# Kernel tuning notes

Measured on AMD Instinct MI355X. Metric: run time of the kernel, lower is better.

## Reference

```python
import jax, jax.numpy as jnp
import numpy as np

B, N = 8, 2048
CLIP, D, BD, NC = 512, 256, 128, 10  # CLIP_EMBED_DIM, GNN_NODE_DIM, BOTTLENECK_DIM_GNN, NUM_CLASSES
LN_EPS = 1e-5


def _layer_norm(x, g, b):
    mu = jnp.mean(x, axis=-1, keepdims=True)
    var = jnp.mean(jnp.square(x - mu), axis=-1, keepdims=True)
    return (x - mu) / jnp.sqrt(var + LN_EPS) * g + b


def setup_inputs() -> dict:
    key = jax.random.key(0)
    ks = jax.random.split(key, 16)
    def w(k, shape, fan_in):
        lim = 1.0 / np.sqrt(fan_in)
        return jax.random.uniform(k, shape, jnp.float32, -lim, lim)
    return {
        "local_feat": jax.random.normal(ks[0], (B, N, CLIP), jnp.float32),
        "coords": jax.random.uniform(ks[1], (B, N, 2), jnp.float32),
        "mask": jax.random.randint(ks[2], (B, N), 0, 2).astype(bool),
        # node_encoder: Linear(CLIP->D) + LayerNorm(D)
        "enc_w": w(ks[3], (CLIP, D), CLIP), "enc_b": jnp.zeros((D,), jnp.float32),
        "enc_g": jnp.ones((D,), jnp.float32), "enc_beta": jnp.zeros((D,), jnp.float32),
        "gamma": jnp.asarray(5.0, jnp.float32),  # spatial_gamma
        "wq": w(ks[4], (D, D), D), "bq": jnp.zeros((D,), jnp.float32),
        "wk": w(ks[5], (D, D), D), "bk": jnp.zeros((D,), jnp.float32),
        "wv": w(ks[6], (D, D), D), "bv": jnp.zeros((D,), jnp.float32),
        # bottleneck: Linear(D->BD) + LayerNorm(BD)
        "bn_w": w(ks[7], (D, BD), D), "bn_b": jnp.zeros((BD,), jnp.float32),
        "bn_g": jnp.ones((BD,), jnp.float32), "bn_beta": jnp.zeros((BD,), jnp.float32),
        # classifier: Linear(BD->BD//2) + ReLU + Linear(BD//2->NC)
        "c1_w": w(ks[8], (BD, BD // 2), BD), "c1_b": jnp.zeros((BD // 2,), jnp.float32),
        "c2_w": w(ks[9], (BD // 2, NC), BD // 2), "c2_b": jnp.zeros((NC,), jnp.float32),
    }


def reference(local_feat, coords, mask, enc_w, enc_b, enc_g, enc_beta, gamma,
              wq, bq, wk, bk, wv, bv, bn_w, bn_b, bn_g, bn_beta,
              c1_w, c1_b, c2_w, c2_b):
    # node encoder: Linear + LN + ReLU -> h [B,N,D]
    h = jax.nn.relu(_layer_norm(local_feat @ enc_w + enc_b, enc_g, enc_beta))
    # pairwise euclidean distances on 2D coords (torch.cdist, under no_grad)
    xy = coords[:, :, :2]
    sq = jnp.sum(xy * xy, axis=-1)                                   # [B,N]
    d2 = sq[:, :, None] + sq[:, None, :] - 2.0 * jnp.einsum('bnd,bmd->bnm', xy, xy)
    dist = jax.lax.stop_gradient(jnp.sqrt(jnp.maximum(d2, 0.0)))     # [B,N,N]
    spatial_adj = jnp.exp(-dist * jnp.abs(gamma))
    q, k, v = h @ wq + bq, h @ wk + bk, h @ wv + bv
    scores = jnp.einsum('bnd,bmd->bnm', q, k) / jnp.sqrt(jnp.float32(D))
    attn = jax.nn.softmax(scores, axis=-1) * spatial_adj             # gated attention
    attn = jnp.where(mask[:, None, :], 0.0, attn)                    # zero masked keys
    agg = jnp.einsum('bnm,bmd->bnd', attn, v)                        # [B,N,D]
    out = jax.nn.relu(_layer_norm(agg @ bn_w + bn_b, bn_g, bn_beta)) # [B,N,BD]
    mask_v = (~mask)[:, :, None].astype(out.dtype)                   # [B,N,1]
    pooled = (out * mask_v).sum(axis=1) / jnp.maximum(mask_v.sum(axis=1), 1e-9)
    logits = jax.nn.relu(pooled @ c1_w + c1_b) @ c2_w + c2_b
    return logits, pooled
```

## Files before the change

### kernel.cpp

```cpp
#include <hip/hip_runtime.h>
#include <hip/hip_bf16.h>

typedef unsigned short ushort_t;
typedef __attribute__((ext_vector_type(8))) short s8;
typedef __attribute__((ext_vector_type(4))) float f4;
typedef __attribute__((ext_vector_type(16))) float f16v;

__device__ __forceinline__ unsigned short f2bf(float f) {
  union { float f; unsigned int u; } c; c.f = f;
  unsigned int r = (c.u + 0x7fffu + ((c.u >> 16) & 1u)) >> 16;
  return (unsigned short)r;
}
__device__ __forceinline__ float bf2f(ushort_t u) {
  union { unsigned int i; float f; } c; c.i = ((unsigned int)u) << 16; return c.f;
}
__device__ __forceinline__ uint4 pack8(float4 a, float4 b) {
  uint4 r;
  r.x = (unsigned)f2bf(a.x) | ((unsigned)f2bf(a.y) << 16);
  r.y = (unsigned)f2bf(a.z) | ((unsigned)f2bf(a.w) << 16);
  r.z = (unsigned)f2bf(b.x) | ((unsigned)f2bf(b.y) << 16);
  r.w = (unsigned)f2bf(b.z) | ((unsigned)f2bf(b.w) << 16);
  return r;
}
__device__ __forceinline__ void dma16(const ushort_t* g, const short* l) {
  __builtin_amdgcn_global_load_lds(
      (const __attribute__((address_space(1))) unsigned int*)g,
      (__attribute__((address_space(3))) unsigned int*)(unsigned long)l,
      16, 0, 0);
}

__global__ __launch_bounds__(256) void k_wt_all(
    const float* __restrict__ enc_w, const float* __restrict__ wq,
    const float* __restrict__ wk, const float* __restrict__ wv,
    const float* __restrict__ bn_w,
    ushort_t* __restrict__ enc_wT, ushort_t* __restrict__ wqkvT,
    ushort_t* __restrict__ bn_wT) {
  const int y = blockIdx.y;
  const int i = blockIdx.x * 256 + threadIdx.x;
  if (y == 0) {
    if (i < 131072) { const int n = i >> 9, k = i & 511; enc_wT[i] = f2bf(enc_w[k * 256 + n]); }
  } else if (y <= 3) {
    if (i < 65536) {
      const int n = i >> 8, k = i & 255;
      const float* src = (y == 1) ? wq : (y == 2) ? wk : wv;
      wqkvT[(y - 1) * 65536 + i] = f2bf(src[k * 256 + n]);
    }
  } else {
    if (i < 32768) { const int n = i >> 8, k = i & 255; bn_wT[i] = f2bf(bn_w[k * 128 + n]); }
  }
}

__global__ __launch_bounds__(256, 3) void k_gemm_enc(
    const float* __restrict__ A, const ushort_t* __restrict__ WT,
    const float* __restrict__ bia, const float* __restrict__ g,
    const float* __restrict__ beta, ushort_t* __restrict__ out) {
  __shared__ short Al[32 * 72];
  __shared__ short Bl[256 * 72];
  __shared__ float red1[32][2], red2[32][2];
  const int t = threadIdx.x;
  const int wv = t >> 6, lane = t & 63, l16 = lane & 15, quad = lane >> 4;
  const int wm = wv >> 1, wn = wv & 1;
  const int row0 = blockIdx.x * 32;

  f4 acc[8];
#pragma unroll
  for (int nf = 0; nf < 8; ++nf) acc[nf] = (f4){0.f, 0.f, 0.f, 0.f};

  for (int k0 = 0; k0 < 512; k0 += 64) {
    __syncthreads();
    {
      const int r = t >> 3, c8 = t & 7;
      const float* src = &A[(size_t)(row0 + r) * 512 + k0 + c8 * 8];
      *(uint4*)&Al[r * 72 + c8 * 8] =
          pack8(*(const float4*)src, *(const float4*)(src + 4));
    }
#pragma unroll
    for (int i = 0; i < 8; ++i) {
      const int ch = t + i * 256;
      const int r = ch >> 3, c8 = ch & 7;
      *(uint4*)&Bl[r * 72 + c8 * 8] =
          *(const uint4*)&WT[(size_t)r * 512 + k0 + c8 * 8];
    }
    __syncthreads();
#pragma unroll
    for (int kc = 0; kc < 2; ++kc) {
      const s8 af = *(const s8*)&Al[(wm * 16 + l16) * 72 + kc * 32 + quad * 8];
#pragma unroll
      for (int nf = 0; nf < 8; ++nf) {
        const s8 bf = *(const s8*)&Bl[(wn * 128 + nf * 16 + l16) * 72 + kc * 32 + quad * 8];
        acc[nf] = __builtin_amdgcn_mfma_f32_16x16x32_bf16(af, bf, acc[nf], 0, 0, 0);
      }
    }
  }
  float bi[8], gg[8], bb[8];
#pragma unroll
  for (int nf = 0; nf < 8; ++nf) {
    const int col = wn * 128 + nf * 16 + l16;
    bi[nf] = bia[col]; gg[nf] = g[col]; bb[nf] = beta[col];
  }
  float s1[4] = {0.f, 0.f, 0.f, 0.f}, s2[4] = {0.f, 0.f, 0.f, 0.f};
#pragma unroll
  for (int nf = 0; nf < 8; ++nf)
#pragma unroll
    for (int r = 0; r < 4; ++r) {
      const float v = acc[nf][r] + bi[nf];
      acc[nf][r] = v;
      s1[r] += v; s2[r] += v * v;
    }
#pragma unroll
  for (int m = 1; m < 16; m <<= 1) {
#pragma unroll
    for (int r = 0; r < 4; ++r) {
      s1[r] += __shfl_xor(s1[r], m);
      s2[r] += __shfl_xor(s2[r], m);
    }
  }
  if (l16 == 0) {
#pragma unroll
    for (int r = 0; r < 4; ++r) {
      const int rl = wm * 16 + quad * 4 + r;
      red1[rl][wn] = s1[r]; red2[rl][wn] = s2[r];
    }
  }
  __syncthreads();
#pragma unroll
  for (int r = 0; r < 4; ++r) {
    const int rl = wm * 16 + quad * 4 + r;
    const float mu = (red1[rl][0] + red1[rl][1]) * (1.f / 256.f);
    const float var = (red2[rl][0] + red2[rl][1]) * (1.f / 256.f) - mu * mu;
    const float rstd = rsqrtf(var + 1e-5f);
#pragma unroll
    for (int nf = 0; nf < 8; ++nf) {
      const int col = wn * 128 + nf * 16 + l16;
      const float v = (acc[nf][r] - mu) * rstd * gg[nf] + bb[nf];
      out[(size_t)(row0 + rl) * 256 + col] = f2bf(fmaxf(v, 0.f));
    }
  }
}

__global__ __launch_bounds__(256, 4) void k_gemm_qkv(
    const ushort_t* __restrict__ A, const ushort_t* __restrict__ WT,
    const float* __restrict__ bq, const float* __restrict__ bk,
    const float* __restrict__ bv,
    ushort_t* __restrict__ q, ushort_t* __restrict__ k, ushort_t* __restrict__ vt) {
  __shared__ short Al[64 * 72];
  __shared__ short Bl[128 * 72];
  const int t = threadIdx.x;
  const int wv = t >> 6, lane = t & 63, l16 = lane & 15, quad = lane >> 4;
  const int wm = wv >> 1, wn = wv & 1;
  const int row0 = blockIdx.x * 64;
  const int nb = blockIdx.y;
  const int type = nb >> 1;
  const ushort_t* wtb = WT + (size_t)nb * 128 * 256;

  f4 acc[2][4];
#pragma unroll
  for (int mf = 0; mf < 2; ++mf)
#pragma unroll
    for (int nf = 0; nf < 4; ++nf) acc[mf][nf] = (f4){0.f, 0.f, 0.f, 0.f};

  for (int k0 = 0; k0 < 256; k0 += 64) {
    __syncthreads();
#pragma unroll
    for (int i = 0; i < 2; ++i) {
      const int ch = t + i * 256;
      const int r = ch >> 3, c8 = ch & 7;
      *(uint4*)&Al[r * 72 + c8 * 8] =
          *(const uint4*)&A[(size_t)(row0 + r) * 256 + k0 + c8 * 8];
    }
#pragma unroll
    for (int i = 0; i < 4; ++i) {
      const int ch = t + i * 256;
      const int r = ch >> 3, c8 = ch & 7;
      *(uint4*)&Bl[r * 72 + c8 * 8] =
          *(const uint4*)&wtb[(size_t)r * 256 + k0 + c8 * 8];
    }
    __syncthreads();
#pragma unroll
    for (int kc = 0; kc < 2; ++kc) {
      s8 af[2];
      af[0] = *(const s8*)&Al[(wm * 32 + l16) * 72 + kc * 32 + quad * 8];
      af[1] = *(const s8*)&Al[(wm * 32 + 16 + l16) * 72 + kc * 32 + quad * 8];
#pragma unroll
      for (int nf = 0; nf < 4; ++nf) {
        const s8 bf = *(const s8*)&Bl[(wn * 64 + nf * 16 + l16) * 72 + kc * 32 + quad * 8];
        acc[0][nf] = __builtin_amdgcn_mfma_f32_16x16x32_bf16(af[0], bf, acc[0][nf], 0, 0, 0);
        acc[1][nf] = __builtin_amdgcn_mfma_f32_16x16x32_bf16(af[1], bf, acc[1][nf], 0, 0, 0);
      }
    }
  }
  const float* bias = (type == 0) ? bq : (type == 1) ? bk : bv;
#pragma unroll
  for (int nf = 0; nf < 4; ++nf) {
    const int colg = nb * 128 + wn * 64 + nf * 16 + l16;
    const int col = colg - type * 256;
    const float bi = bias[col];
    if (type == 2) {
      const int b = row0 >> 11;
#pragma unroll
      for (int mf = 0; mf < 2; ++mf) {
        const int n = (row0 & 2047) + wm * 32 + mf * 16 + quad * 4;
        ushort4 pk;
        pk.x = f2bf(acc[mf][nf][0] + bi);
        pk.y = f2bf(acc[mf][nf][1] + bi);
        pk.z = f2bf(acc[mf][nf][2] + bi);
        pk.w = f2bf(acc[mf][nf][3] + bi);
        *(ushort4*)&vt[((size_t)b * 256 + col) * 2048 + n] = pk;
      }
    } else {
      ushort_t* dst = (type == 0) ? q : k;
      const float sc = (type == 0) ? 0.0625f : 1.f;
#pragma unroll
      for (int mf = 0; mf < 2; ++mf)
#pragma unroll
        for (int r = 0; r < 4; ++r) {
          const int row = row0 + wm * 32 + mf * 16 + quad * 4 + r;
          dst[(size_t)row * 256 + col] = f2bf((acc[mf][nf][r] + bi) * sc);
        }
    }
  }
}

__global__ __launch_bounds__(256, 2) void k_attn(
    const ushort_t* __restrict__ qb, const ushort_t* __restrict__ kb,
    const ushort_t* __restrict__ vtb,
    const float* __restrict__ coords, const int* __restrict__ mask,
    const float* __restrict__ gam,
    ushort_t* __restrict__ Opb, float* __restrict__ lws) {
  __shared__ short kld[2][8192];
  __shared__ short vld[2][8192];
  __shared__ short pl[128 * 40];
  const int t = threadIdx.x;
  const int wv = t >> 6, lane = t & 63, l16 = lane & 15, quad = lane >> 4;
  const int hw = lane >> 5, l32 = lane & 31;
  const int b = blockIdx.z, ks = blockIdx.y;
  const int qw = blockIdx.x * 128 + wv * 32;
  const int kbase = ks * 512;

  float rcx[2][4], rcy[2][4];
#pragma unroll
  for (int mf = 0; mf < 2; ++mf)
#pragma unroll
    for (int r = 0; r < 4; ++r) {
      const float2 cc = ((const float2*)coords)[b * 2048 + qw + mf * 16 + quad * 4 + r];
      rcx[mf][r] = cc.x; rcy[mf][r] = cc.y;
    }
  const float gamma = fabsf(gam[0]);

  f16v o32[8];
#pragma unroll
  for (int i = 0; i < 8; ++i)
#pragma unroll
    for (int j = 0; j < 16; ++j) o32[i][j] = 0.f;
  float lrun[2][4];
#pragma unroll
  for (int mf = 0; mf < 2; ++mf)
#pragma unroll
    for (int r = 0; r < 4; ++r) lrun[mf][r] = 0.f;

  const ushort_t* kbb = kb + ((size_t)b * 2048 + kbase) * 256;
  const ushort_t* vbb = vtb + (size_t)b * 256 * 2048 + kbase;
  const ushort_t* qrow0 = qb + ((size_t)b * 2048 + qw + l16) * 256 + quad * 8;
  const ushort_t* qrow1 = qrow0 + 16 * 256;

#pragma unroll
  for (int i = 0; i < 4; ++i) {
    const int i2 = wv * 4 + i;
    dma16(kbb + (size_t)l32 * 256 + (i2 * 2 + hw) * 8, &kld[0][i2 * 512]);
    dma16(vbb + (size_t)(i * 64 + lane) * 2048 + wv * 8, &vld[0][(wv * 256 + i * 64) * 8]);
  }
  __syncthreads();

  for (int kt = 0; kt < 16; ++kt) {
    const int cur = kt & 1;
    const int m0 = kbase + kt * 32;
    if (kt < 15) {
      const ushort_t* kn = kbb + (size_t)(kt + 1) * 32 * 256;
      const ushort_t* vn = vbb + (kt + 1) * 32;
      const int nb2 = cur ^ 1;
#pragma unroll
      for (int i = 0; i < 4; ++i) {
        const int i2 = wv * 4 + i;
        dma16(kn + (size_t)l32 * 256 + (i2 * 2 + hw) * 8, &kld[nb2][i2 * 512]);
        dma16(vn + (size_t)(i * 64 + lane) * 2048 + wv * 8, &vld[nb2][(wv * 256 + i * 64) * 8]);
      }
    }
    f4 sc[2][2];
#pragma unroll
    for (int mf = 0; mf < 2; ++mf)
#pragma unroll
      for (int s = 0; s < 2; ++s) sc[mf][s] = (f4){0.f, 0.f, 0.f, 0.f};
#pragma unroll
    for (int c = 0; c < 8; ++c) {
      const s8 qa0 = *(const s8*)(qrow0 + c * 32);
      const s8 qa1 = *(const s8*)(qrow1 + c * 32);
#pragma unroll
      for (int s = 0; s < 2; ++s) {
        const s8 bfr = *(const s8*)&kld[cur][((c * 4 + quad) * 32 + s * 16 + l16) * 8];
        sc[0][s] = __builtin_amdgcn_mfma_f32_16x16x32_bf16(qa0, bfr, sc[0][s], 0, 0, 0);
        sc[1][s] = __builtin_amdgcn_mfma_f32_16x16x32_bf16(qa1, bfr, sc[1][s], 0, 0, 0);
      }
    }
#pragma unroll
    for (int s = 0; s < 2; ++s) {
      const int m = m0 + s * 16 + l16;
      const float2 cc = ((const float2*)coords)[b * 2048 + m];
      const float mfv = mask[b * 2048 + m] ? 0.f : 1.f;
#pragma unroll
      for (int mf = 0; mf < 2; ++mf)
#pragma unroll
        for (int r = 0; r < 4; ++r) {
          const float p = __expf(sc[mf][s][r]);
          lrun[mf][r] += p;
          const float dx = rcx[mf][r] - cc.x, dy = rcy[mf][r] - cc.y;
          const float dist = sqrtf(fmaxf(dx * dx + dy * dy, 0.f));
          const float w = p * __expf(-gamma * dist) * mfv;
          pl[(wv * 32 + mf * 16 + quad * 4 + r) * 40 + s * 16 + l16] = (short)f2bf(w);
        }
    }
    const s8 pa0 = *(const s8*)&pl[(wv * 32 + l32) * 40 + hw * 8];
    const s8 pa1 = *(const s8*)&pl[(wv * 32 + l32) * 40 + 16 + hw * 8];
#pragma unroll
    for (int dt = 0; dt < 8; ++dt) {
      const s8 bv0 = *(const s8*)&vld[cur][(hw * 256 + dt * 32 + l32) * 8];
      o32[dt] = __builtin_amdgcn_mfma_f32_32x32x16_bf16(pa0, bv0, o32[dt], 0, 0, 0);
      const s8 bv1 = *(const s8*)&vld[cur][((2 + hw) * 256 + dt * 32 + l32) * 8];
      o32[dt] = __builtin_amdgcn_mfma_f32_32x32x16_bf16(pa1, bv1, o32[dt], 0, 0, 0);
    }
    __syncthreads();
  }
  ushort_t* OpK = Opb + (size_t)ks * 4194304;
#pragma unroll
  for (int dt = 0; dt < 8; ++dt) {
#pragma unroll
    for (int reg = 0; reg < 16; ++reg) {
      const int row = (reg & 3) + 8 * (reg >> 2) + 4 * hw;
      OpK[((size_t)b * 2048 + qw + row) * 256 + dt * 32 + l32] = f2bf(o32[dt][reg]);
    }
  }
#pragma unroll
  for (int o2 = 1; o2 < 16; o2 <<= 1) {
#pragma unroll
    for (int mf = 0; mf < 2; ++mf)
#pragma unroll
      for (int r = 0; r < 4; ++r) lrun[mf][r] += __shfl_xor(lrun[mf][r], o2);
  }
  if (l16 == 0) {
#pragma unroll
    for (int mf = 0; mf < 2; ++mf)
#pragma unroll
      for (int r = 0; r < 4; ++r)
        lws[ks * 16384 + b * 2048 + qw + mf * 16 + quad * 4 + r] = lrun[mf][r];
  }
}

__global__ __launch_bounds__(256, 3) void k_gemm_bn(
    const ushort_t* __restrict__ Opb, const float* __restrict__ lws,
    const ushort_t* __restrict__ WT,
    const float* __restrict__ bia, const float* __restrict__ g,
    const float* __restrict__ beta, float* __restrict__ pooledAcc) {
  __shared__ short Al[32 * 72];
  __shared__ short Bl[128 * 72];
  __shared__ float red1[32][2], red2[32][2];
  __shared__ float sCm[32];
  const int t = threadIdx.x;
  const int wv = t >> 6, lane = t & 63, l16 = lane & 15, quad = lane >> 4;
  const int wm = wv >> 1, wn = wv & 1;
  const int row0 = blockIdx.x * 32;
  const int b = row0 >> 11;

  if (t < 32) {
    const int row = row0 + t;
    sCm[t] = 1.f / (lws[row] + lws[16384 + row] + lws[32768 + row] + lws[49152 + row]);
  }

  f4 acc[4];
#pragma unroll
  for (int nf = 0; nf < 4; ++nf) acc[nf] = (f4){0.f, 0.f, 0.f, 0.f};

  for (int k0 = 0; k0 < 256; k0 += 64) {
    __syncthreads();
    {
      const int r = t >> 3, c8 = t & 7;
      const float c0 = sCm[r];
      const size_t off = (size_t)(row0 + r) * 256 + k0 + c8 * 8;
      float e[8];
#pragma unroll
      for (int j = 0; j < 8; ++j) e[j] = 0.f;
#pragma unroll
      for (int pp = 0; pp < 4; ++pp) {
        const uint4 u = *(const uint4*)&Opb[(size_t)pp * 4194304 + off];
        e[0] += bf2f((ushort_t)(u.x & 0xffff)); e[1] += bf2f((ushort_t)(u.x >> 16));
        e[2] += bf2f((ushort_t)(u.y & 0xffff)); e[3] += bf2f((ushort_t)(u.y >> 16));
        e[4] += bf2f((ushort_t)(u.z & 0xffff)); e[5] += bf2f((ushort_t)(u.z >> 16));
        e[6] += bf2f((ushort_t)(u.w & 0xffff)); e[7] += bf2f((ushort_t)(u.w >> 16));
      }
      float4 ea = {c0 * e[0], c0 * e[1], c0 * e[2], c0 * e[3]};
      float4 eb = {c0 * e[4], c0 * e[5], c0 * e[6], c0 * e[7]};
      *(uint4*)&Al[r * 72 + c8 * 8] = pack8(ea, eb);
    }
#pragma unroll
    for (int i = 0; i < 4; ++i) {
      const int ch = t + i * 256;
      const int r = ch >> 3, c8 = ch & 7;
      *(uint4*)&Bl[r * 72 + c8 * 8] =
          *(const uint4*)&WT[(size_t)r * 256 + k0 + c8 * 8];
    }
    __syncthreads();
#pragma unroll
    for (int kc = 0; kc < 2; ++kc) {
      const s8 af = *(const s8*)&Al[(wm * 16 + l16) * 72 + kc * 32 + quad * 8];
#pragma unroll
      for (int nf = 0; nf < 4; ++nf) {
        const s8 bf = *(const s8*)&Bl[(wn * 64 + nf * 16 + l16) * 72 + kc * 32 + quad * 8];
        acc[nf] = __builtin_amdgcn_mfma_f32_16x16x32_bf16(af, bf, acc[nf], 0, 0, 0);
      }
    }
  }
  float bi[4], gg[4], bb[4];
#pragma unroll
  for (int nf = 0; nf < 4; ++nf) {
    const int col = wn * 64 + nf * 16 + l16;
    bi[nf] = bia[col]; gg[nf] = g[col]; bb[nf] = beta[col];
  }
  float s1[4] = {0.f, 0.f, 0.f, 0.f}, s2[4] = {0.f, 0.f, 0.f, 0.f};
#pragma unroll
  for (int nf = 0; nf < 4; ++nf)
#pragma unroll
    for (int r = 0; r < 4; ++r) {
      const float v = acc[nf][r] + bi[nf];
      acc[nf][r] = v;
      s1[r] += v; s2[r] += v * v;
    }
#pragma unroll
  for (int m = 1; m < 16; m <<= 1) {
#pragma unroll
    for (int r = 0; r < 4; ++r) {
      s1[r] += __shfl_xor(s1[r], m);
      s2[r] += __shfl_xor(s2[r], m);
    }
  }
  if (l16 == 0) {
#pragma unroll
    for (int r = 0; r < 4; ++r) {
      const int rl = wm * 16 + quad * 4 + r;
      red1[rl][wn] = s1[r]; red2[rl][wn] = s2[r];
    }
  }
  __syncthreads();
  float colsum[4] = {0.f, 0.f, 0.f, 0.f};
  const int* mrow = (const int*)0;
#pragma unroll
  for (int r = 0; r < 4; ++r) {
    const int rl = wm * 16 + quad * 4 + r;
    const float mu = (red1[rl][0] + red1[rl][1]) * (1.f / 128.f);
    const float var = (red2[rl][0] + red2[rl][1]) * (1.f / 128.f) - mu * mu;
    const float rstd = rsqrtf(var + 1e-5f);
    extern const int* __mask_dummy;
#pragma unroll
    for (int nf = 0; nf < 4; ++nf) {
      const float v = (acc[nf][r] - mu) * rstd * gg[nf] + bb[nf];
      acc[nf][r] = fmaxf(v, 0.f);
    }
  }
  (void)mrow;
  {
    float mw[4];
#pragma unroll
    for (int r = 0; r < 4; ++r) {
      const int rl = wm * 16 + quad * 4 + r;
      mw[r] = pooledAcc[1024 + row0 + rl] ;
    }
#pragma unroll
    for (int nf = 0; nf < 4; ++nf) {
      float s = acc[nf][0] * mw[0] + acc[nf][1] * mw[1] +
                acc[nf][2] * mw[2] + acc[nf][3] * mw[3];
      s += __shfl_xor(s, 16);
      s += __shfl_xor(s, 32);
      if (quad == 0) {
        const int col = wn * 64 + nf * 16 + l16;
        atomicAdd(&pooledAcc[b * 128 + col], s);
      }
    }
  }
}

__global__ __launch_bounds__(256) void k_maskf(const int* __restrict__ mask,
                                               float* __restrict__ pooledAcc) {
  const int i = blockIdx.x * 256 + threadIdx.x;
  if (i < 16384) pooledAcc[1024 + i] = mask[i] ? 0.f : 1.f;
  if (i < 1024) pooledAcc[i] = 0.f;
}

__global__ __launch_bounds__(128) void k_pool2_head(
    const float* __restrict__ pooledAcc, const int* __restrict__ mask,
    const float* __restrict__ c1w, const float* __restrict__ c1b,
    const float* __restrict__ c2w, const float* __restrict__ c2b,
    float* __restrict__ dout) {
  __shared__ float ps[128];
  __shared__ float h1[64];
  __shared__ float scnt[128];
  const int b = blockIdx.x, t = threadIdx.x;
  float c = 0.f;
  const int* mb = mask + b * 2048 + t * 16;
#pragma unroll
  for (int j = 0; j < 16; ++j) c += mb[j] ? 0.f : 1.f;
  scnt[t] = c;
  __syncthreads();
  for (int o2 = 64; o2 > 0; o2 >>= 1) {
    if (t < o2) scnt[t] += scnt[t + o2];
    __syncthreads();
  }
  const float cnt = scnt[0];
  const float p = pooledAcc[b * 128 + t] / fmaxf(cnt, 1e-9f);
  ps[t] = p;
  dout[80 + b * 128 + t] = p;
  __syncthreads();
  if (t < 64) {
    float acc = c1b[t];
    for (int d = 0; d < 128; ++d) acc += ps[d] * c1w[d * 64 + t];
    h1[t] = fmaxf(acc, 0.f);
  }
  __syncthreads();
  if (t < 10) {
    float a2 = c2b[t];
    for (int j = 0; j < 64; ++j) a2 += h1[j] * c2w[j * 10 + t];
    dout[b * 10 + t] = a2;
  }
}

extern "C" void kernel_launch(void* const* d_in, const int* in_sizes, int n_in,
                              void* d_out, int out_size, void* d_ws, size_t ws_size,
                              hipStream_t stream) {
  const float* lf     = (const float*)d_in[0];
  const float* coords = (const float*)d_in[1];
  const int*   mask   = (const int*)d_in[2];
  const float* enc_w  = (const float*)d_in[3];
  const float* enc_b  = (const float*)d_in[4];
  const float* enc_g  = (const float*)d_in[5];
  const float* enc_be = (const float*)d_in[6];
  const float* gamma  = (const float*)d_in[7];
  const float* wq     = (const float*)d_in[8];
  const float* bq     = (const float*)d_in[9];
  const float* wk     = (const float*)d_in[10];
  const float* bk     = (const float*)d_in[11];
  const float* wv     = (const float*)d_in[12];
  const float* bv     = (const float*)d_in[13];
  const float* bn_w   = (const float*)d_in[14];
  const float* bn_b   = (const float*)d_in[15];
  const float* bn_g   = (const float*)d_in[16];
  const float* bn_be  = (const float*)d_in[17];
  const float* c1w    = (const float*)d_in[18];
  const float* c1b    = (const float*)d_in[19];
  const float* c2w    = (const float*)d_in[20];
  const float* c2b    = (const float*)d_in[21];

  float* ws = (float*)d_ws;
  ushort_t* h_bf   = (ushort_t*)ws;
  ushort_t* q_bf   = (ushort_t*)(ws + 2097152);
  ushort_t* k_bf   = (ushort_t*)(ws + 4194304);
  ushort_t* vt_bf  = (ushort_t*)(ws + 6291456);
  ushort_t* Opb    = (ushort_t*)(ws + 8388608);
  ushort_t* enc_wT = (ushort_t*)(ws + 17825792);
  ushort_t* wqkvT  = (ushort_t*)(ws + 17891328);
  ushort_t* bn_wT  = (ushort_t*)(ws + 17989632);
  float*    lws    = ws + 18006016;
  float*    pooledAcc = ws + 18071552;
  float* out = (float*)d_out;

  k_wt_all<<<dim3(512, 5), 256, 0, stream>>>(enc_w, wq, wk, wv, bn_w,
                                             enc_wT, wqkvT, bn_wT);
  k_maskf<<<64, 256, 0, stream>>>(mask, pooledAcc);
  k_gemm_enc<<<512, 256, 0, stream>>>(lf, enc_wT, enc_b, enc_g, enc_be, h_bf);
  k_gemm_qkv<<<dim3(256, 6), 256, 0, stream>>>(h_bf, wqkvT, bq, bk, bv, q_bf, k_bf, vt_bf);
  k_attn<<<dim3(16, 4, 8), 256, 0, stream>>>(q_bf, k_bf, vt_bf, coords, mask, gamma,
                                             Opb, lws);
  k_gemm_bn<<<512, 256, 0, stream>>>(Opb, lws, bn_wT, bn_b, bn_g, bn_be, pooledAcc);
  k_pool2_head<<<8, 128, 0, stream>>>(pooledAcc, mask, c1w, c1b, c2w, c2b, out);
}
```

Before: 257.9 us.

## Keep attention probabilities in registers by transposing score MFMA, dropping LDS staging

The QK^T MFMA swaps operands so each lane holds scores for one query row across consecutive keys. That lets the gated softmax weights be packed straight into bf16 MFMA A-fragments for the PV product (now 16x16x32 tiles), which removes the shared-memory round trip for P. Key coordinates and mask are loaded as vectors, Q fragments are hoisted per tile, and sqrt uses the raw v_sqrt instruction. The trade is more accumulator fragments and possibly higher register pressure, plus a changed output store pattern.

```diff
diff --git a/kernel.cpp b/kernel.cpp
--- a/kernel.cpp
+++ b/kernel.cpp
@@ -2,6 +2,7 @@
 #include <hip/hip_bf16.h>
 
 typedef unsigned short ushort_t;
+typedef __attribute__((ext_vector_type(4))) short s4;
 typedef __attribute__((ext_vector_type(8))) short s8;
 typedef __attribute__((ext_vector_type(4))) float f4;
 typedef __attribute__((ext_vector_type(16))) float f16v;
@@ -21,6 +22,9 @@
   r.z = (unsigned)f2bf(b.x) | ((unsigned)f2bf(b.y) << 16);
   r.w = (unsigned)f2bf(b.z) | ((unsigned)f2bf(b.w) << 16);
   return r;
+}
+__device__ __forceinline__ float fsqrt_fast(float x) {
+  float r; asm("v_sqrt_f32 %0, %1" : "=v"(r) : "v"(x)); return r;
 }
 __device__ __forceinline__ void dma16(const ushort_t* g, const short* l) {
   __builtin_amdgcn_global_load_lds(
@@ -229,7 +233,6 @@
     ushort_t* __restrict__ Opb, float* __restrict__ lws) {
   __shared__ short kld[2][8192];
   __shared__ short vld[2][8192];
-  __shared__ short pl[128 * 40];
   const int t = threadIdx.x;
   const int wv = t >> 6, lane = t & 63, l16 = lane & 15, quad = lane >> 4;
   const int hw = lane >> 5, l32 = lane & 31;
@@ -237,26 +240,20 @@
   const int qw = blockIdx.x * 128 + wv * 32;
   const int kbase = ks * 512;
 
-  float rcx[2][4], rcy[2][4];
+  float rcx[2], rcy[2];
+  {
+    const float2 c0 = ((const float2*)coords)[b * 2048 + qw + l16];
+    const float2 c1 = ((const float2*)coords)[b * 2048 + qw + 16 + l16];
+    rcx[0] = c0.x; rcy[0] = c0.y; rcx[1] = c1.x; rcy[1] = c1.y;
+  }
+  const float gamma = fabsf(gam[0]);
+
+  f4 o[2][16];
 #pragma unroll
   for (int mf = 0; mf < 2; ++mf)
 #pragma unroll
-    for (int r = 0; r < 4; ++r) {
-      const float2 cc = ((const float2*)coords)[b * 2048 + qw + mf * 16 + quad * 4 + r];
-      rcx[mf][r] = cc.x; rcy[mf][r] = cc.y;
-    }
-  const float gamma = fabsf(gam[0]);
-
-  f16v o32[8];
-#pragma unroll
-  for (int i = 0; i < 8; ++i)
-#pragma unroll
-    for (int j = 0; j < 16; ++j) o32[i][j] = 0.f;
-  float lrun[2][4];
-#pragma unroll
-  for (int mf = 0; mf < 2; ++mf)
-#pragma unroll
-    for (int r = 0; r < 4; ++r) lrun[mf][r] = 0.f;
+    for (int dt = 0; dt < 16; ++dt) o[mf][dt] = (f4){0.f, 0.f, 0.f, 0.f};
+  float lrun[2] = {0.f, 0.f};
 
   const ushort_t* kbb = kb + ((size_t)b * 2048 + kbase) * 256;
   const ushort_t* vbb = vtb + (size_t)b * 256 * 2048 + kbase;
@@ -274,6 +271,20 @@
   for (int kt = 0; kt < 16; ++kt) {
     const int cur = kt & 1;
     const int m0 = kbase + kt * 32;
+
+    s8 qa[2][8];
+#pragma unroll
+    for (int c = 0; c < 8; ++c) {
+      qa[0][c] = *(const s8*)(qrow0 + c * 32);
+      qa[1][c] = *(const s8*)(qrow1 + c * 32);
+    }
+    const float4 kca = *(const float4*)&coords[((size_t)b * 2048 + m0 + quad * 4) * 2];
+    const float4 kcb = *(const float4*)&coords[((size_t)b * 2048 + m0 + quad * 4) * 2 + 4];
+    const float4 kcc = *(const float4*)&coords[((size_t)b * 2048 + m0 + 16 + quad * 4) * 2];
+    const float4 kcd = *(const float4*)&coords[((size_t)b * 2048 + m0 + 16 + quad * 4) * 2 + 4];
+    const int4 mq0 = *(const int4*)&mask[b * 2048 + m0 + quad * 4];
+    const int4 mq1 = *(const int4*)&mask[b * 2048 + m0 + 16 + quad * 4];
+
     if (kt < 15) {
       const ushort_t* kn = kbb + (size_t)(kt + 1) * 32 * 256;
       const ushort_t* vn = vbb + (kt + 1) * 32;
@@ -285,6 +296,7 @@
         dma16(vn + (size_t)(i * 64 + lane) * 2048 + wv * 8, &vld[nb2][(wv * 256 + i * 64) * 8]);
       }
     }
+
     f4 sc[2][2];
 #pragma unroll
     for (int mf = 0; mf < 2; ++mf)
@@ -292,65 +304,73 @@
       for (int s = 0; s < 2; ++s) sc[mf][s] = (f4){0.f, 0.f, 0.f, 0.f};
 #pragma unroll
     for (int c = 0; c < 8; ++c) {
-      const s8 qa0 = *(const s8*)(qrow0 + c * 32);
-      const s8 qa1 = *(const s8*)(qrow1 + c * 32);
 #pragma unroll
       for (int s = 0; s < 2; ++s) {
-        const s8 bfr = *(const s8*)&kld[cur][((c * 4 + quad) * 32 + s * 16 + l16) * 8];
-        sc[0][s] = __builtin_amdgcn_mfma_f32_16x16x32_bf16(qa0, bfr, sc[0][s], 0, 0, 0);
-        sc[1][s] = __builtin_amdgcn_mfma_f32_16x16x32_bf16(qa1, bfr, sc[1][s], 0, 0, 0);
-      }
-    }
-#pragma unroll
-    for (int s = 0; s < 2; ++s) {
-      const int m = m0 + s * 16 + l16;
-      const float2 cc = ((const float2*)coords)[b * 2048 + m];
-      const float mfv = mask[b * 2048 + m] ? 0.f : 1.f;
-#pragma unroll
-      for (int mf = 0; mf < 2; ++mf)
-#pragma unroll
-        for (int r = 0; r < 4; ++r) {
-          const float p = __expf(sc[mf][s][r]);
-          lrun[mf][r] += p;
-          const float dx = rcx[mf][r] - cc.x, dy = rcy[mf][r] - cc.y;
-          const float dist = sqrtf(fmaxf(dx * dx + dy * dy, 0.f));
-          const float w = p * __expf(-gamma * dist) * mfv;
-          pl[(wv * 32 + mf * 16 + quad * 4 + r) * 40 + s * 16 + l16] = (short)f2bf(w);
+        const s8 kf = *(const s8*)&kld[cur][((c * 4 + quad) * 32 + s * 16 + l16) * 8];
+        sc[0][s] = __builtin_amdgcn_mfma_f32_16x16x32_bf16(kf, qa[0][c], sc[0][s], 0, 0, 0);
+        sc[1][s] = __builtin_amdgcn_mfma_f32_16x16x32_bf16(kf, qa[1][c], sc[1][s], 0, 0, 0);
+      }
+    }
+
+    const float kx[8] = {kca.x, kca.z, kcb.x, kcb.z, kcc.x, kcc.z, kcd.x, kcd.z};
+    const float ky[8] = {kca.y, kca.w, kcb.y, kcb.w, kcc.y, kcc.w, kcd.y, kcd.w};
+    const int  mk[8] = {mq0.x, mq0.y, mq0.z, mq0.w, mq1.x, mq1.y, mq1.z, mq1.w};
+    s8 paf[2];
+#pragma unroll
+    for (int mf = 0; mf < 2; ++mf) {
+      unsigned pu[4];
+#pragma unroll
+      for (int s = 0; s < 2; ++s) {
+#pragma unroll
+        for (int rp = 0; rp < 2; ++rp) {
+          float wp[2];
+#pragma unroll
+          for (int e = 0; e < 2; ++e) {
+            const int r = rp * 2 + e;
+            const int j = s * 4 + r;
+            const float p = __expf(sc[mf][s][r]);
+            lrun[mf] += p;
+            const float dx = rcx[mf] - kx[j], dy = rcy[mf] - ky[j];
+            const float dist = fsqrt_fast(dx * dx + dy * dy);
+            wp[e] = mk[j] ? 0.f : p * __expf(-gamma * dist);
+          }
+          pu[s * 2 + rp] = (unsigned)f2bf(wp[0]) | ((unsigned)f2bf(wp[1]) << 16);
         }
-    }
-    const s8 pa0 = *(const s8*)&pl[(wv * 32 + l32) * 40 + hw * 8];
-    const s8 pa1 = *(const s8*)&pl[(wv * 32 + l32) * 40 + 16 + hw * 8];
-#pragma unroll
-    for (int dt = 0; dt < 8; ++dt) {
-      const s8 bv0 = *(const s8*)&vld[cur][(hw * 256 + dt * 32 + l32) * 8];
-      o32[dt] = __builtin_amdgcn_mfma_f32_32x32x16_bf16(pa0, bv0, o32[dt], 0, 0, 0);
-      const s8 bv1 = *(const s8*)&vld[cur][((2 + hw) * 256 + dt * 32 + l32) * 8];
-      o32[dt] = __builtin_amdgcn_mfma_f32_32x32x16_bf16(pa1, bv1, o32[dt], 0, 0, 0);
+      }
+      union { s8 v; unsigned u[4]; } cv;
+      cv.u[0] = pu[0]; cv.u[1] = pu[1]; cv.u[2] = pu[2]; cv.u[3] = pu[3];
+      paf[mf] = cv.v;
+    }
+
+#pragma unroll
+    for (int dt = 0; dt < 16; ++dt) {
+      const int base = ((quad >> 1) * 256 + dt * 16 + l16) * 8 + (quad & 1) * 4;
+      const s4 lo = *(const s4*)&vld[cur][base];
+      const s4 hi = *(const s4*)&vld[cur][base + 4096];
+      const s8 bvf = __builtin_shufflevector(lo, hi, 0, 1, 2, 3, 4, 5, 6, 7);
+      o[0][dt] = __builtin_amdgcn_mfma_f32_16x16x32_bf16(paf[0], bvf, o[0][dt], 0, 0, 0);
+      o[1][dt] = __builtin_amdgcn_mfma_f32_16x16x32_bf16(paf[1], bvf, o[1][dt], 0, 0, 0);
     }
     __syncthreads();
   }
   ushort_t* OpK = Opb + (size_t)ks * 4194304;
 #pragma unroll
-  for (int dt = 0; dt < 8; ++dt) {
-#pragma unroll
-    for (int reg = 0; reg < 16; ++reg) {
-      const int row = (reg & 3) + 8 * (reg >> 2) + 4 * hw;
-      OpK[((size_t)b * 2048 + qw + row) * 256 + dt * 32 + l32] = f2bf(o32[dt][reg]);
-    }
-  }
-#pragma unroll
-  for (int o2 = 1; o2 < 16; o2 <<= 1) {
-#pragma unroll
-    for (int mf = 0; mf < 2; ++mf)
-#pragma unroll
-      for (int r = 0; r < 4; ++r) lrun[mf][r] += __shfl_xor(lrun[mf][r], o2);
-  }
-  if (l16 == 0) {
-#pragma unroll
-    for (int mf = 0; mf < 2; ++mf)
+  for (int mf = 0; mf < 2; ++mf)
+#pragma unroll
+    for (int dt = 0; dt < 16; ++dt)
 #pragma unroll
       for (int r = 0; r < 4; ++r)
-        lws[ks * 16384 + b * 2048 + qw + mf * 16 + quad * 4 + r] = lrun[mf][r];
+        OpK[((size_t)b * 2048 + qw + mf * 16 + quad * 4 + r) * 256 + dt * 16 + l16] =
+            f2bf(o[mf][dt][r]);
+
+#pragma unroll
+  for (int mf = 0; mf < 2; ++mf) {
+    lrun[mf] += __shfl_xor(lrun[mf], 16);
+    lrun[mf] += __shfl_xor(lrun[mf], 32);
+  }
+  if (quad == 0) {
+    lws[ks * 16384 + b * 2048 + qw + l16] = lrun[0];
+    lws[ks * 16384 + b * 2048 + qw + 16 + l16] = lrun[1];
   }
 }
 
@@ -448,28 +468,24 @@
     }
   }
   __syncthreads();
-  float colsum[4] = {0.f, 0.f, 0.f, 0.f};
-  const int* mrow = (const int*)0;
 #pragma unroll
   for (int r = 0; r < 4; ++r) {
     const int rl = wm * 16 + quad * 4 + r;
     const float mu = (red1[rl][0] + red1[rl][1]) * (1.f / 128.f);
     const float var = (red2[rl][0] + red2[rl][1]) * (1.f / 128.f) - mu * mu;
     const float rstd = rsqrtf(var + 1e-5f);
-    extern const int* __mask_dummy;
 #pragma unroll
     for (int nf = 0; nf < 4; ++nf) {
       const float v = (acc[nf][r] - mu) * rstd * gg[nf] + bb[nf];
       acc[nf][r] = fmaxf(v, 0.f);
     }
   }
-  (void)mrow;
   {
     float mw[4];
 #pragma unroll
     for (int r = 0; r < 4; ++r) {
       const int rl = wm * 16 + quad * 4 + r;
-      mw[r] = pooledAcc[1024 + row0 + rl] ;
+      mw[r] = pooledAcc[1024 + row0 + rl];
     }
 #pragma unroll
     for (int nf = 0; nf < 4; ++nf) {
```

After: 257.6 us. About the same (-0.1%).
